# Optimization experiments

Measured on AMD Instinct MI355X. Metric: run time of the kernel, lower is better.

## Reference

```python
import jax, jax.numpy as jnp
import numpy as np

VOCAB, EMBED, HIDDEN = 32000, 256, 512
B, S = 64, 64


def setup_inputs() -> dict:
    key = jax.random.key(0)
    ks = jax.random.split(key, 10)
    target_seq = jax.random.randint(ks[0], (B, S), 0, VOCAB)
    context = jax.random.normal(ks[1], (B, HIDDEN), dtype=jnp.float32)
    h = jax.random.normal(ks[2], (B, HIDDEN), dtype=jnp.float32)
    c = jax.random.normal(ks[3], (B, HIDDEN), dtype=jnp.float32)
    # parameters (torch default-ish init scale)
    emb_table = jax.random.normal(ks[4], (VOCAB, EMBED), dtype=jnp.float32)
    k_lstm = 1.0 / np.sqrt(HIDDEN)
    w_ih = jax.random.uniform(ks[5], (4 * HIDDEN, EMBED + HIDDEN), minval=-k_lstm, maxval=k_lstm, dtype=jnp.float32)
    w_hh = jax.random.uniform(ks[6], (4 * HIDDEN, HIDDEN), minval=-k_lstm, maxval=k_lstm, dtype=jnp.float32)
    b_ih = jax.random.uniform(ks[7], (4 * HIDDEN,), minval=-k_lstm, maxval=k_lstm, dtype=jnp.float32)
    b_hh = jnp.zeros((4 * HIDDEN,), dtype=jnp.float32)
    k_fc = 1.0 / np.sqrt(2 * HIDDEN)
    w_fc = jax.random.uniform(ks[8], (VOCAB, 2 * HIDDEN), minval=-k_fc, maxval=k_fc, dtype=jnp.float32)
    b_fc = jax.random.uniform(ks[9], (VOCAB,), minval=-k_fc, maxval=k_fc, dtype=jnp.float32)
    return dict(target_seq=target_seq, context=context, h=h, c=c,
                emb_table=emb_table, w_ih=w_ih, w_hh=w_hh, b_ih=b_ih, b_hh=b_hh,
                w_fc=w_fc, b_fc=b_fc)


def _decode(target_seq, context, h, c, emb_table, w_ih, w_hh, b_ih, b_hh, w_fc, b_fc):
    # teacher_forcing_ratio = 1.0 -> input at step t is target_seq[:, t]
    emb = emb_table[target_seq]                                    # [B,S,E]
    ctx_t = jnp.broadcast_to(context[:, None, :], (emb.shape[0], emb.shape[1], context.shape[1]))
    lstm_in = jnp.concatenate([emb, ctx_t], axis=-1)               # [B,S,E+H]
    # precompute input-to-hidden part of gates for all steps
    pre = jnp.einsum('bsf,gf->bsg', lstm_in, w_ih) + b_ih + b_hh   # [B,S,4H]
    H = h.shape[1]

    def step(carry, pre_t):
        h_t, c_t = carry
        gates = pre_t + h_t @ w_hh.T                               # [B,4H]
        i, f, g, o = jnp.split(gates, 4, axis=-1)
        i, f, o = jax.nn.sigmoid(i), jax.nn.sigmoid(f), jax.nn.sigmoid(o)
        g = jnp.tanh(g)
        c_n = f * c_t + i * g
        h_n = o * jnp.tanh(c_n)
        return (h_n, c_n), h_n

    _, hs = jax.lax.scan(step, (h, c), jnp.swapaxes(pre, 0, 1))    # hs: [S,B,H]
    hs = jnp.swapaxes(hs, 0, 1)                                    # [B,S,H]
    out_in = jnp.concatenate([hs, ctx_t], axis=-1)                 # [B,S,2H]
    logits = jnp.einsum('bsf,vf->bsv', out_in, w_fc) + b_fc        # [B,S,V]
    return logits


def reference(target_seq, context, h, c, emb_table, w_ih, w_hh, b_ih, b_hh, w_fc, b_fc):
    return _decode(target_seq, context, h, c, emb_table, w_ih, w_hh, b_ih, b_hh, w_fc, b_fc)
```

## Files before the change

kernel.cpp:

```cpp
#include <hip/hip_runtime.h>
#include <hip/hip_bf16.h>

#define VOCAB 32000
#define EMBED 256
#define HIDDEN 512
#define BB 64
#define SS 64
#define M_ROWS (BB * SS)
#define G4 (4 * HIDDEN)
#define NBLK 16
#define NTOT 256
#define NTILE_N (VOCAB / 256)
#define NTILE_M (M_ROWS / 256)

typedef __attribute__((ext_vector_type(8))) short short8v;
typedef __attribute__((ext_vector_type(4))) float float4v;
typedef __attribute__((ext_vector_type(4))) unsigned int uint4v;

__device__ __forceinline__ ushort f2bf(float f) {
    union { float f; unsigned u; } v; v.f = f;
    unsigned r = (v.u + 0x7FFFu + ((v.u >> 16) & 1u)) >> 16;
    return (ushort)r;
}

__device__ __forceinline__ float fast_tanh(float x) {
    float xc = fminf(fmaxf(x, -15.f), 15.f);
    float e = __expf(2.f * xc);
    return (e - 1.f) / (e + 1.f);
}

__device__ __forceinline__ void glds16(const ushort* g, ushort* l) {
    __builtin_amdgcn_global_load_lds(
        (const __attribute__((address_space(1))) unsigned int*)(const void*)g,
        (__attribute__((address_space(3))) unsigned int*)(void*)l, 16, 0, 0);
}

__global__ void k_conv_strided(const float* __restrict__ in, ushort* __restrict__ out,
                               int lg2cols, int instride, int n8) {
    int i = blockIdx.x * blockDim.x + threadIdx.x;
    int stride = gridDim.x * blockDim.x;
    int colmask = (1 << lg2cols) - 1;
    for (; i < n8; i += stride) {
        int i8 = i << 3;
        int row = i8 >> lg2cols, col = i8 & colmask;
        const float* src = in + (size_t)row * instride + col;
        float4 v0 = *(const float4*)src;
        float4 v1 = *(const float4*)(src + 4);
        short8v o;
        o[0] = (short)f2bf(v0.x); o[1] = (short)f2bf(v0.y);
        o[2] = (short)f2bf(v0.z); o[3] = (short)f2bf(v0.w);
        o[4] = (short)f2bf(v1.x); o[5] = (short)f2bf(v1.y);
        o[6] = (short)f2bf(v1.z); o[7] = (short)f2bf(v1.w);
        *(short8v*)(out + i8) = o;
    }
}

__global__ void k_build_emb(const int* __restrict__ tseq, const float* __restrict__ emb,
                            ushort* __restrict__ embbf) {
    int rid = blockIdx.x * 8 + (threadIdx.x >> 5);
    int c0 = (threadIdx.x & 31) * 8;
    int tok = tseq[rid];
    const float* src = emb + (size_t)tok * EMBED + c0;
    float4 v0 = *(const float4*)src;
    float4 v1 = *(const float4*)(src + 4);
    short8v o;
    o[0] = (short)f2bf(v0.x); o[1] = (short)f2bf(v0.y);
    o[2] = (short)f2bf(v0.z); o[3] = (short)f2bf(v0.w);
    o[4] = (short)f2bf(v1.x); o[5] = (short)f2bf(v1.y);
    o[6] = (short)f2bf(v1.z); o[7] = (short)f2bf(v1.w);
    *(short8v*)(embbf + (size_t)rid * EMBED + c0) = o;
}

__global__ void k_prep_small(const float* __restrict__ b_ih, const float* __restrict__ b_hh,
                             float* __restrict__ bias_pre,
                             const float* __restrict__ h0, ushort* __restrict__ hbufA,
                             const float* __restrict__ ctx, ushort* __restrict__ ctx_bf,
                             unsigned* __restrict__ ctrl) {
    int i = blockIdx.x * blockDim.x + threadIdx.x;
    if (i < 1024) ctrl[i] = 0;
    if (i < G4) bias_pre[i] = b_ih[i] + b_hh[i];
    if (i < BB * HIDDEN) {
        hbufA[i] = f2bf(h0[i]);
        ctx_bf[i] = f2bf(ctx[i]);
    }
}

__global__ __launch_bounds__(256) void k_gemm_smallM(
    const ushort* __restrict__ Abf, const float* __restrict__ Wf, int wstride,
    const float* __restrict__ bias, float* __restrict__ Cout, int N) {
    int t = threadIdx.x;
    int wv = t >> 6, lane = t & 63, lr = lane & 15, kg = lane >> 4;
    int bcol = blockIdx.x * 128;

    float4v acc[4][2];
#pragma unroll
    for (int m = 0; m < 4; m++)
#pragma unroll
        for (int n = 0; n < 2; n++) acc[m][n] = (float4v){0.f, 0.f, 0.f, 0.f};

#pragma unroll 4
    for (int ks = 0; ks < 16; ks++) {
        short8v a[4];
#pragma unroll
        for (int m = 0; m < 4; m++)
            a[m] = *(const short8v*)(Abf + (size_t)(m * 16 + lr) * 512 + ks * 32 + kg * 8);
        short8v w[2];
#pragma unroll
        for (int n = 0; n < 2; n++) {
            const float* src = Wf + (size_t)(bcol + wv * 32 + n * 16 + lr) * wstride + ks * 32 + kg * 8;
            float4 v0 = *(const float4*)src;
            float4 v1 = *(const float4*)(src + 4);
            short8v w8;
            w8[0] = (short)f2bf(v0.x); w8[1] = (short)f2bf(v0.y);
            w8[2] = (short)f2bf(v0.z); w8[3] = (short)f2bf(v0.w);
            w8[4] = (short)f2bf(v1.x); w8[5] = (short)f2bf(v1.y);
            w8[6] = (short)f2bf(v1.z); w8[7] = (short)f2bf(v1.w);
            w[n] = w8;
        }
#pragma unroll
        for (int m = 0; m < 4; m++)
#pragma unroll
            for (int n = 0; n < 2; n++)
                acc[m][n] = __builtin_amdgcn_mfma_f32_16x16x32_bf16(a[m], w[n], acc[m][n], 0, 0, 0);
    }

#pragma unroll
    for (int n = 0; n < 2; n++) {
        int col = bcol + wv * 32 + n * 16 + lr;
        float bv = bias[col];
#pragma unroll
        for (int m = 0; m < 4; m++) {
            int row = m * 16 + kg * 4;
#pragma unroll
            for (int j = 0; j < 4; j++)
                Cout[(size_t)(row + j) * N + col] = acc[m][n][j] + bv;
        }
    }
}

__global__ __launch_bounds__(512) void k_gemm_bf16(
    const ushort* __restrict__ A, const ushort* __restrict__ W,
    const float* __restrict__ rowbias, float* __restrict__ C,
    int M, int N, int K) {
    __shared__ ushort As[256 * 32];
    __shared__ ushort Ws[256 * 32];
    int t = threadIdx.x;

    int gx = N >> 8, gy = M >> 8;
    int nwg = gx * gy;
    int q = nwg >> 3, r = nwg & 7;
    int xcd = blockIdx.x & 7, idx = blockIdx.x >> 3;
    int wg = (xcd < r) ? xcd * (q + 1) + idx : r * (q + 1) + (xcd - r) * q + idx;
    const int SG = 4;
    int grp = wg / (gx * SG);
    int rem = wg % (gx * SG);
    int bx = rem / SG;
    int by = grp * SG + rem % SG;
    int brow = by * 256, bcol = bx * 256;

    int wave = t >> 6, lane = t & 63;
    int wr = wave >> 2, wc = wave & 3;
    int lr = lane & 15, kg = lane >> 4;

    float4v acc[8][4];
#pragma unroll
    for (int m = 0; m < 8; m++)
#pragma unroll
        for (int n = 0; n < 4; n++) acc[m][n] = (float4v){0.f, 0.f, 0.f, 0.f};

    int srow = t >> 2;
    int scol = (((t & 3) ^ (srow & 3))) * 8;
    const ushort* AgA = A + (size_t)(brow + srow) * K + scol;
    const ushort* AgB = A + (size_t)(brow + 128 + srow) * K + scol;
    const ushort* WgA = W + (size_t)(bcol + srow) * K + scol;
    const ushort* WgB = W + (size_t)(bcol + 128 + srow) * K + scol;
    ushort* ldsA0 = &As[(wave * 16) * 32];
    ushort* ldsA1 = &As[(128 + wave * 16) * 32];
    ushort* ldsW0 = &Ws[(wave * 16) * 32];
    ushort* ldsW1 = &Ws[(128 + wave * 16) * 32];

    for (int bk = 0; bk < K; bk += 32) {
        glds16(AgA + bk, ldsA0);
        glds16(AgB + bk, ldsA1);
        glds16(WgA + bk, ldsW0);
        glds16(WgB + bk, ldsW1);
        __syncthreads();
        short8v a[8], w[4];
#pragma unroll
        for (int m = 0; m < 8; m++) {
            int row = wr * 128 + m * 16 + lr;
            a[m] = *(const short8v*)&As[row * 32 + (kg ^ (row & 3)) * 8];
        }
#pragma unroll
        for (int n = 0; n < 4; n++) {
            int row = wc * 64 + n * 16 + lr;
            w[n] = *(const short8v*)&Ws[row * 32 + (kg ^ (row & 3)) * 8];
        }
#pragma unroll
        for (int m = 0; m < 8; m++)
#pragma unroll
            for (int n = 0; n < 4; n++)
                acc[m][n] = __builtin_amdgcn_mfma_f32_16x16x32_bf16(a[m], w[n], acc[m][n], 0, 0, 0);
        __syncthreads();
    }

#pragma unroll
    for (int n = 0; n < 4; n++) {
        int col = bcol + wc * 64 + n * 16 + lr;
#pragma unroll
        for (int m = 0; m < 8; m++) {
            int row = brow + wr * 128 + m * 16 + kg * 4;
            float bv = rowbias[(size_t)(row >> 6) * N + col];
            float4v v = acc[m][n];
#pragma unroll
            for (int j = 0; j < 4; j++)
                C[(size_t)(row + j) * N + col] = v[j] + bv;
        }
    }
}

__global__ __launch_bounds__(512) void k_mega(
    const float* __restrict__ pre, const float* __restrict__ w_hh,
    const float* __restrict__ c0,
    ushort* __restrict__ hbufA, ushort* __restrict__ hbufB,
    ushort* __restrict__ out_in, unsigned* __restrict__ ctrl,
    const ushort* __restrict__ Wfc, const float* __restrict__ ctxdot,
    float* __restrict__ Cout) {
    __shared__ __align__(16) char smem[99328];
    __shared__ int s_tile;
    unsigned* flags = ctrl;
    unsigned* queue = ctrl + 512;
    int t = threadIdx.x;
    int bid = blockIdx.x;
    int wave = t >> 6, lane = t & 63, lr = lane & 15, kg = lane >> 4;

    if (bid < NBLK) {
        ushort* h_lds = (ushort*)smem;
        float* G2 = (float*)(smem + 65536);
        char* hl = (char*)h_lds;
        int p = bid;
        int w = wave;
        int mh = w >> 2, cw2 = w & 3;

        short8v wfrag[2][16];
#pragma unroll
        for (int ci = 0; ci < 2; ci++) {
            const float* wrow = w_hh + (size_t)(cw2 * HIDDEN + p * 32 + ci * 16 + lr) * HIDDEN;
#pragma unroll
            for (int ks = 0; ks < 16; ks++) {
                const float* src = wrow + ks * 32 + kg * 8;
                short8v w8;
#pragma unroll
                for (int e = 0; e < 8; e++) w8[e] = (short)f2bf(src[e]);
                wfrag[ci][ks] = w8;
            }
        }

        int b = t >> 3, jj0 = (t & 7) * 4, jg0 = p * 32 + jj0;
        float4v c_reg = *(const float4v*)(c0 + (size_t)b * HIDDEN + jg0);
        float4v pv[4];
#pragma unroll
        for (int qg = 0; qg < 4; qg++)
            pv[qg] = *(const float4v*)(pre + (size_t)(b * SS) * G4 + qg * HIDDEN + jg0);

        for (int s = 0; s < SS; s++) {
            const ushort* hb = (s & 1) ? hbufB : hbufA;
            ushort* hn = (s & 1) ? hbufA : hbufB;

            if (s > 0) {
                const unsigned* fp = flags + (lane & 15) * 16;
                unsigned fv;
                do {
                    fv = __hip_atomic_load(fp, __ATOMIC_RELAXED, __HIP_MEMORY_SCOPE_AGENT);
                } while (__all((int)(fv >= (unsigned)s)) == 0);
            }

            {
                uint4v vb[8];
#pragma unroll
                for (int i = 0; i < 8; i++) {
                    int rr = w * 8 + i;
                    const void* src = hb + (size_t)rr * HIDDEN + lane * 8;
                    asm volatile("global_load_dwordx4 %0, %1, off sc0 sc1"
                                 : "=&v"(vb[i]) : "v"(src));
                }
                asm volatile("s_waitcnt vmcnt(0)" ::: "memory");
#pragma unroll
                for (int i = 0; i < 8; i++) {
                    int rr = w * 8 + i;
                    int off = (rr * 1024 + lane * 16) ^ ((rr & 7) << 4);
                    *(uint4v*)(hl + off) = vb[i];
                }
            }
            __syncthreads();

            float4v acc[2][2];
#pragma unroll
            for (int mi = 0; mi < 2; mi++)
#pragma unroll
                for (int ci = 0; ci < 2; ci++) acc[mi][ci] = (float4v){0.f, 0.f, 0.f, 0.f};
#pragma unroll
            for (int ks = 0; ks < 16; ks++) {
                short8v a[2];
#pragma unroll
                for (int mi = 0; mi < 2; mi++) {
                    int row = mh * 32 + mi * 16 + lr;
                    int off = (row * 1024 + ks * 64 + kg * 16) ^ ((row & 7) << 4);
                    a[mi] = *(const short8v*)(hl + off);
                }
#pragma unroll
                for (int mi = 0; mi < 2; mi++)
#pragma unroll
                    for (int ci = 0; ci < 2; ci++)
                        acc[mi][ci] = __builtin_amdgcn_mfma_f32_16x16x32_bf16(a[mi], wfrag[ci][ks], acc[mi][ci], 0, 0, 0);
            }
#pragma unroll
            for (int mi = 0; mi < 2; mi++)
#pragma unroll
                for (int ci = 0; ci < 2; ci++)
#pragma unroll
                    for (int rr = 0; rr < 4; rr++)
                        G2[(mh * 32 + mi * 16 + kg * 4 + rr) * 132 + cw2 * 32 + ci * 16 + lr] = acc[mi][ci][rr];
            __syncthreads();

            {
                float4v gq[4];
#pragma unroll
                for (int qg = 0; qg < 4; qg++) gq[qg] = *(const float4v*)&G2[b * 132 + qg * 32 + jj0];
                unsigned long long hv8 = 0;
#pragma unroll
                for (int e = 0; e < 4; e++) {
                    float xi = gq[0][e] + pv[0][e];
                    float xf = gq[1][e] + pv[1][e];
                    float xg = gq[2][e] + pv[2][e];
                    float xo = gq[3][e] + pv[3][e];
                    float ig = 1.f / (1.f + __expf(-xi));
                    float fg = 1.f / (1.f + __expf(-xf));
                    float gg = fast_tanh(xg);
                    float og = 1.f / (1.f + __expf(-xo));
                    float cn = fg * c_reg[e] + ig * gg;
                    float hv = og * fast_tanh(cn);
                    c_reg[e] = cn;
                    hv8 |= (unsigned long long)f2bf(hv) << (16 * e);
                }
                if (s + 1 < SS) {
                    __hip_atomic_store((unsigned long long*)(hn + (size_t)b * HIDDEN + jg0), hv8,
                                       __ATOMIC_RELAXED, __HIP_MEMORY_SCOPE_AGENT);
                }
                __hip_atomic_store((unsigned long long*)(out_in + (size_t)(s * BB + b) * HIDDEN + jg0), hv8,
                                   __ATOMIC_RELAXED, __HIP_MEMORY_SCOPE_AGENT);
                if (s + 1 < SS) {
#pragma unroll
                    for (int qg = 0; qg < 4; qg++)
                        pv[qg] = *(const float4v*)(pre + (size_t)(b * SS + s + 1) * G4 + qg * HIDDEN + jg0);
                }
            }

            __syncthreads();
            if (t == 0)
                __hip_atomic_store(flags + p * 16, (unsigned)(s + 1),
                                   __ATOMIC_RELEASE, __HIP_MEMORY_SCOPE_AGENT);
        }
    } else {
        ushort* As = (ushort*)smem;
        ushort* Ws = (ushort*)(smem + 16384);
        int wr = wave >> 2, wc = wave & 3;
        int srow = t >> 2;
        int scol = ((t & 3) ^ (srow & 3)) * 8;
        ushort* ldsA0 = As + (wave * 16) * 32;
        ushort* ldsA1 = As + (128 + wave * 16) * 32;
        ushort* ldsW0 = Ws + (wave * 16) * 32;
        ushort* ldsW1 = Ws + (128 + wave * 16) * 32;

        for (;;) {
            __syncthreads();
            if (t == 0)
                s_tile = (int)__hip_atomic_fetch_add(queue, 1u, __ATOMIC_RELAXED, __HIP_MEMORY_SCOPE_AGENT);
            __syncthreads();
            int tile = s_tile;
            if (tile >= NTILE_M * NTILE_N) break;
            int mt = tile / NTILE_N, nt = tile % NTILE_N;
            int brow = mt * 256, bcol = nt * 256;

            {
                unsigned need = (unsigned)(4 * mt + 4);
                const unsigned* fp = flags + (lane & 15) * 16;
                unsigned fv;
                do {
                    fv = __hip_atomic_load(fp, __ATOMIC_RELAXED, __HIP_MEMORY_SCOPE_AGENT);
                } while (__all((int)(fv >= need)) == 0);
                (void)__hip_atomic_load(flags, __ATOMIC_ACQUIRE, __HIP_MEMORY_SCOPE_AGENT);
            }

            float4v acc[8][4];
#pragma unroll
            for (int m = 0; m < 8; m++)
#pragma unroll
                for (int n = 0; n < 4; n++) acc[m][n] = (float4v){0.f, 0.f, 0.f, 0.f};

            const ushort* AgA = out_in + (size_t)(brow + srow) * HIDDEN + scol;
            const ushort* AgB = AgA + (size_t)128 * HIDDEN;
            const ushort* WgA = Wfc + (size_t)(bcol + srow) * HIDDEN + scol;
            const ushort* WgB = WgA + (size_t)128 * HIDDEN;

            for (int bk = 0; bk < HIDDEN; bk += 32) {
                glds16(AgA + bk, ldsA0);
                glds16(AgB + bk, ldsA1);
                glds16(WgA + bk, ldsW0);
                glds16(WgB + bk, ldsW1);
                __syncthreads();
                short8v a[8], w[4];
#pragma unroll
                for (int m = 0; m < 8; m++) {
                    int row = wr * 128 + m * 16 + lr;
                    a[m] = *(const short8v*)&As[row * 32 + (kg ^ (row & 3)) * 8];
                }
#pragma unroll
                for (int n = 0; n < 4; n++) {
                    int row = wc * 64 + n * 16 + lr;
                    w[n] = *(const short8v*)&Ws[row * 32 + (kg ^ (row & 3)) * 8];
                }
#pragma unroll
                for (int m = 0; m < 8; m++)
#pragma unroll
                    for (int n = 0; n < 4; n++)
                        acc[m][n] = __builtin_amdgcn_mfma_f32_16x16x32_bf16(a[m], w[n], acc[m][n], 0, 0, 0);
                __syncthreads();
            }

#pragma unroll
            for (int n = 0; n < 4; n++) {
                int col = bcol + wc * 64 + n * 16 + lr;
#pragma unroll
                for (int m = 0; m < 8; m++) {
                    int rbase = wr * 128 + m * 16 + kg * 4;
#pragma unroll
                    for (int j = 0; j < 4; j++) {
                        int rl = rbase + j;
                        int bb = rl & 63;
                        int ss = mt * 4 + (rl >> 6);
                        Cout[(size_t)(bb * 64 + ss) * VOCAB + col] =
                            acc[m][n][j] + ctxdot[(size_t)bb * VOCAB + col];
                    }
                }
            }
        }
    }
}

extern "C" void kernel_launch(void* const* d_in, const int* in_sizes, int n_in,
                              void* d_out, int out_size, void* d_ws, size_t ws_size,
                              hipStream_t stream) {
    const int*   tseq = (const int*)d_in[0];
    const float* ctx  = (const float*)d_in[1];
    const float* h0   = (const float*)d_in[2];
    const float* c0   = (const float*)d_in[3];
    const float* emb  = (const float*)d_in[4];
    const float* w_ih = (const float*)d_in[5];
    const float* w_hh = (const float*)d_in[6];
    const float* b_ih = (const float*)d_in[7];
    const float* b_hh = (const float*)d_in[8];
    const float* w_fc = (const float*)d_in[9];
    const float* b_fc = (const float*)d_in[10];
    float* out = (float*)d_out;

    char* wsb = (char*)d_ws;
    size_t off = 0;
    auto alloc = [&](size_t bytes) -> void* {
        void* ptr = wsb + off;
        off = (off + bytes + 255) & ~(size_t)255;
        return ptr;
    };
    ushort* emb_bf    = (ushort*)alloc((size_t)M_ROWS * EMBED * 2);
    ushort* w_ih_ebf  = (ushort*)alloc((size_t)G4 * EMBED * 2);
    ushort* w_fc_hbf  = (ushort*)alloc((size_t)VOCAB * HIDDEN * 2);
    ushort* out_in    = (ushort*)alloc((size_t)M_ROWS * HIDDEN * 2);
    float*  pre       = (float*)alloc((size_t)M_ROWS * G4 * 4);
    float*  prectx    = (float*)alloc((size_t)BB * G4 * 4);
    float*  ctxdot    = (float*)alloc((size_t)BB * VOCAB * 4);
    ushort* ctx_bf    = (ushort*)alloc((size_t)BB * HIDDEN * 2);
    ushort* hbufA     = (ushort*)alloc((size_t)BB * HIDDEN * 2);
    ushort* hbufB     = (ushort*)alloc((size_t)BB * HIDDEN * 2);
    float*  bias_pre  = (float*)alloc((size_t)G4 * 4);
    unsigned* ctrl    = (unsigned*)alloc(4096);

    k_conv_strided<<<256, 256, 0, stream>>>(w_ih, w_ih_ebf, 8, 768, G4 * EMBED / 8);
    k_conv_strided<<<2048, 256, 0, stream>>>(w_fc, w_fc_hbf, 9, 1024, VOCAB * HIDDEN / 8);
    k_build_emb<<<M_ROWS / 8, 256, 0, stream>>>(tseq, emb, emb_bf);
    k_prep_small<<<128, 256, 0, stream>>>(b_ih, b_hh, bias_pre, h0, hbufA, ctx, ctx_bf, ctrl);

    k_gemm_smallM<<<G4 / 128, 256, 0, stream>>>(ctx_bf, w_ih + 256, 768, bias_pre, prectx, G4);
    k_gemm_smallM<<<VOCAB / 128, 256, 0, stream>>>(ctx_bf, w_fc + 512, 1024, b_fc, ctxdot, VOCAB);

    k_gemm_bf16<<<dim3((G4 / 256) * (M_ROWS / 256)), 512, 0, stream>>>(
        emb_bf, w_ih_ebf, prectx, pre, M_ROWS, G4, EMBED);

    void* args[] = {(void*)&pre, (void*)&w_hh, (void*)&c0,
                    (void*)&hbufA, (void*)&hbufB, (void*)&out_in, (void*)&ctrl,
                    (void*)&w_fc_hbf, (void*)&ctxdot, (void*)&out};
    hipLaunchCooperativeKernel((void*)k_mega, dim3(NTOT), dim3(512), args, 0, stream);
}
```

Baseline: 771.2 us.

## Double-buffer FC GEMM tiles with register-staged A loads and cached flag gating

Rewrites the FC GEMM K-loop into a double-buffered pipeline. The next K slice of W is prefetched to LDS via glds16 and the next A slice is prefetched into registers with coherent (sc0 sc1) global loads while MFMAs run on the current buffer. Only wave 0 now polls the progress flags, with s_sleep backoff, and the wait is skipped when an earlier tile already gated the same step. The intent is to hide global-load latency behind compute and cut polling traffic, at the cost of doubled LDS, more registers and hand-placed waitcnt/barrier asm that must stay correct.

```diff
diff --git a/kernel.cpp b/kernel.cpp
--- a/kernel.cpp
+++ b/kernel.cpp
@@ -362,15 +362,16 @@
                                    __ATOMIC_RELEASE, __HIP_MEMORY_SCOPE_AGENT);
         }
     } else {
-        ushort* As = (ushort*)smem;
-        ushort* Ws = (ushort*)(smem + 16384);
+        ushort* Asb = (ushort*)smem;
+        ushort* Wsb = (ushort*)(smem + 32768);
         int wr = wave >> 2, wc = wave & 3;
         int srow = t >> 2;
         int scol = ((t & 3) ^ (srow & 3)) * 8;
-        ushort* ldsA0 = As + (wave * 16) * 32;
-        ushort* ldsA1 = As + (128 + wave * 16) * 32;
-        ushort* ldsW0 = Ws + (wave * 16) * 32;
-        ushort* ldsW1 = Ws + (128 + wave * 16) * 32;
+        int aoff0 = srow * 32 + (t & 3) * 8;
+        int aoff1 = aoff0 + 128 * 32;
+        int woff0 = (wave * 16) * 32;
+        int woff1 = (128 + wave * 16) * 32;
+        int last_gated = -1;
 
         for (;;) {
             __syncthreads();
@@ -382,14 +383,18 @@
             int mt = tile / NTILE_N, nt = tile % NTILE_N;
             int brow = mt * 256, bcol = nt * 256;
 
-            {
-                unsigned need = (unsigned)(4 * mt + 4);
-                const unsigned* fp = flags + (lane & 15) * 16;
-                unsigned fv;
-                do {
-                    fv = __hip_atomic_load(fp, __ATOMIC_RELAXED, __HIP_MEMORY_SCOPE_AGENT);
-                } while (__all((int)(fv >= need)) == 0);
-                (void)__hip_atomic_load(flags, __ATOMIC_ACQUIRE, __HIP_MEMORY_SCOPE_AGENT);
+            int need = 4 * mt + 4;
+            if (need > last_gated) {
+                if (wave == 0) {
+                    const unsigned* fp = flags + (lane & 15) * 16;
+                    for (;;) {
+                        unsigned fv = __hip_atomic_load(fp, __ATOMIC_RELAXED, __HIP_MEMORY_SCOPE_AGENT);
+                        if (__all((int)(fv >= (unsigned)need))) break;
+                        asm volatile("s_sleep 32");
+                    }
+                }
+                __syncthreads();
+                last_gated = need;
             }
 
             float4v acc[8][4];
@@ -398,35 +403,62 @@
 #pragma unroll
                 for (int n = 0; n < 4; n++) acc[m][n] = (float4v){0.f, 0.f, 0.f, 0.f};
 
-            const ushort* AgA = out_in + (size_t)(brow + srow) * HIDDEN + scol;
-            const ushort* AgB = AgA + (size_t)128 * HIDDEN;
-            const ushort* WgA = Wfc + (size_t)(bcol + srow) * HIDDEN + scol;
-            const ushort* WgB = WgA + (size_t)128 * HIDDEN;
-
-            for (int bk = 0; bk < HIDDEN; bk += 32) {
-                glds16(AgA + bk, ldsA0);
-                glds16(AgB + bk, ldsA1);
-                glds16(WgA + bk, ldsW0);
-                glds16(WgB + bk, ldsW1);
-                __syncthreads();
-                short8v a[8], w[4];
-#pragma unroll
-                for (int m = 0; m < 8; m++) {
-                    int row = wr * 128 + m * 16 + lr;
-                    a[m] = *(const short8v*)&As[row * 32 + (kg ^ (row & 3)) * 8];
-                }
-#pragma unroll
-                for (int n = 0; n < 4; n++) {
-                    int row = wc * 64 + n * 16 + lr;
-                    w[n] = *(const short8v*)&Ws[row * 32 + (kg ^ (row & 3)) * 8];
-                }
-#pragma unroll
-                for (int m = 0; m < 8; m++)
-#pragma unroll
-                    for (int n = 0; n < 4; n++)
-                        acc[m][n] = __builtin_amdgcn_mfma_f32_16x16x32_bf16(a[m], w[n], acc[m][n], 0, 0, 0);
-                __syncthreads();
-            }
+            const ushort* Ag  = out_in + (size_t)(brow + srow) * HIDDEN + scol;
+            const ushort* Ag2 = Ag + (size_t)128 * HIDDEN;
+            const ushort* Wg  = Wfc + (size_t)(bcol + srow) * HIDDEN + scol;
+            const ushort* Wg2 = Wg + (size_t)128 * HIDDEN;
+
+            uint4v vaA0, vaA1, vaB0, vaB1;
+            asm volatile("global_load_dwordx4 %0, %1, off sc0 sc1" : "=&v"(vaA0) : "v"((const void*)Ag));
+            asm volatile("global_load_dwordx4 %0, %1, off sc0 sc1" : "=&v"(vaA1) : "v"((const void*)Ag2));
+            glds16(Wg, Wsb + woff0);
+            glds16(Wg2, Wsb + woff1);
+
+#define MEGA_STEP(K, VA0, VA1, VB0, VB1, CUR, NXT)                                            \
+            {                                                                                  \
+                const int bk = (K) * 32;                                                       \
+                if ((K) < 15) {                                                                \
+                    asm volatile("global_load_dwordx4 %0, %1, off sc0 sc1"                     \
+                                 : "=&v"(VB0) : "v"((const void*)(Ag + bk + 32)));             \
+                    asm volatile("global_load_dwordx4 %0, %1, off sc0 sc1"                     \
+                                 : "=&v"(VB1) : "v"((const void*)(Ag2 + bk + 32)));            \
+                    glds16(Wg + bk + 32, Wsb + (NXT) * 8192 + woff0);                          \
+                    glds16(Wg2 + bk + 32, Wsb + (NXT) * 8192 + woff1);                         \
+                    asm volatile("s_waitcnt vmcnt(4)" ::: "memory");                           \
+                } else {                                                                       \
+                    asm volatile("s_waitcnt vmcnt(0)" ::: "memory");                           \
+                }                                                                              \
+                *(uint4v*)(Asb + (CUR) * 8192 + aoff0) = VA0;                                  \
+                *(uint4v*)(Asb + (CUR) * 8192 + aoff1) = VA1;                                  \
+                asm volatile("s_waitcnt lgkmcnt(0)" ::: "memory");                             \
+                asm volatile("s_barrier" ::: "memory");                                        \
+                const ushort* Asc = Asb + (CUR) * 8192;                                        \
+                const ushort* Wsc = Wsb + (CUR) * 8192;                                        \
+                short8v a_[8], w_[4];                                                          \
+                _Pragma("unroll")                                                              \
+                for (int m = 0; m < 8; m++) {                                                  \
+                    int row = wr * 128 + m * 16 + lr;                                          \
+                    a_[m] = *(const short8v*)&Asc[row * 32 + (kg ^ (row & 3)) * 8];            \
+                }                                                                              \
+                _Pragma("unroll")                                                              \
+                for (int n = 0; n < 4; n++) {                                                  \
+                    int row = wc * 64 + n * 16 + lr;                                           \
+                    w_[n] = *(const short8v*)&Wsc[row * 32 + (kg ^ (row & 3)) * 8];            \
+                }                                                                              \
+                _Pragma("unroll")                                                              \
+                for (int m = 0; m < 8; m++)                                                    \
+                    _Pragma("unroll")                                                          \
+                    for (int n = 0; n < 4; n++)                                                \
+                        acc[m][n] = __builtin_amdgcn_mfma_f32_16x16x32_bf16(a_[m], w_[n], acc[m][n], 0, 0, 0); \
+                asm volatile("s_barrier" ::: "memory");                                        \
+            }
+
+#pragma unroll
+            for (int kk = 0; kk < 8; kk++) {
+                MEGA_STEP(2 * kk,     vaA0, vaA1, vaB0, vaB1, 0, 1)
+                MEGA_STEP(2 * kk + 1, vaB0, vaB1, vaA0, vaA1, 1, 0)
+            }
+#undef MEGA_STEP
 
 #pragma unroll
             for (int n = 0; n < 4; n++) {
```

Measured after the change: 665.9 us. -13.7%, faster.
